# Optimization experiments

Hardware: AMD Instinct MI355X
Metric: run time of the kernel (lower is better)

## Reference

```python
import jax, jax.numpy as jnp
import numpy as np
from jax import lax

N, C, K = 400000, 64, 27  # points, channels, 3x3x3 kernel offsets


def setup_inputs() -> dict:
    key = jax.random.key(0)
    ks = jax.random.split(key, 7)
    scale = 1.0 / np.sqrt(C * K)
    x = jax.random.normal(ks[0], (N, C), dtype=jnp.float32)
    W0 = jax.random.normal(ks[1], (K, C, C), dtype=jnp.float32) * scale
    b0 = jax.random.normal(ks[2], (C,), dtype=jnp.float32) * 0.01
    W1 = jax.random.normal(ks[3], (K, C, C), dtype=jnp.float32) * scale
    b1 = jax.random.normal(ks[4], (C,), dtype=jnp.float32) * 0.01
    # stride-1 conv: input/output coordinate sets coincide -> shared neighbor map
    neighbor_idx = jax.random.randint(ks[5], (N, K), 0, N, dtype=jnp.int32)
    neighbor_mask = jax.random.bernoulli(ks[6], 0.5, (N, K))  # bool, missing neighbors masked
    return {"x": x, "W0": W0, "b0": b0, "W1": W1, "b1": b1,
            "neighbor_idx": neighbor_idx, "neighbor_mask": neighbor_mask}


def _sparse_conv(x, W, b, neighbor_idx, neighbor_mask):
    # gather-GEMM-scatter, accumulated over the K=27 kernel offsets via scan
    # x: [N,C], W: [K,C,C], neighbor_idx/mask: [N,K]
    def body(acc, inputs):
        w_k, idx_k, m_k = inputs  # [C,C], [N], [N]
        g = x[idx_k] * m_k.astype(x.dtype)[:, None]  # masked gather [N,C]
        return acc + g @ w_k, None

    acc0 = jnp.zeros_like(x)
    acc, _ = lax.scan(body, acc0, (W, neighbor_idx.T, neighbor_mask.T))
    return acc + b


def reference(x, W0, b0, W1, b1, neighbor_idx, neighbor_mask):
    out = jax.nn.relu(_sparse_conv(x, W0, b0, neighbor_idx, neighbor_mask))
    out = _sparse_conv(out, W1, b1, neighbor_idx, neighbor_mask)
    return out + x  # residual add
```

## Files before the change

### kernel.cpp

```cpp
#include <hip/hip_runtime.h>
#include <stdint.h>

typedef __attribute__((ext_vector_type(8))) short short8;
typedef __attribute__((ext_vector_type(4))) float floatx4;
typedef __attribute__((ext_vector_type(4))) int int4v;
typedef __attribute__((ext_vector_type(4))) short short4v;

#define NPTS 400000
#define KOFF 27

__device__ __forceinline__ unsigned short f2bf(float v) {
    union { float f; unsigned int u; } a; a.f = v;
    unsigned int r = a.u + 0x7FFFu + ((a.u >> 16) & 1u);
    return (unsigned short)(r >> 16);
}

__global__ __launch_bounds__(256) void cvt_x_kernel(const float* __restrict__ x,
                                                    unsigned short* __restrict__ xb,
                                                    int n4) {
    int t = blockIdx.x * 256 + threadIdx.x;
    if (t >= n4) return;
    floatx4 v = *(const floatx4*)(x + (size_t)t * 4);
    short4v o;
#pragma unroll
    for (int j = 0; j < 4; ++j) o[j] = (short)f2bf(v[j]);
    *(short4v*)(xb + (size_t)t * 4) = o;
}

__global__ __launch_bounds__(256) void pack_kernel(const int* __restrict__ idx,
                                                   const int* __restrict__ msk,
                                                   int* __restrict__ pk, int n4) {
    int t = blockIdx.x * 256 + threadIdx.x;
    if (t >= n4) return;
    int4v a = *(const int4v*)(idx + (size_t)t * 4);
    int4v m = *(const int4v*)(msk + (size_t)t * 4);
    int4v o;
#pragma unroll
    for (int j = 0; j < 4; ++j) o[j] = a[j] | (m[j] ? (int)0x80000000 : 0);
    *(int4v*)(pk + (size_t)t * 4) = o;
}

__global__ __launch_bounds__(256) void cvt_w_kernel(const float* __restrict__ W,
                                                    unsigned short* __restrict__ wb) {
    int t = blockIdx.x * 256 + threadIdx.x;
    int k = t >> 12, cout = (t >> 6) & 63, cin = t & 63;
    wb[t] = f2bf(W[(k << 12) + (cin << 6) + cout]);
}

template <int LAYER>
__global__ __launch_bounds__(256, 4) void conv_layer(
        const unsigned short* __restrict__ xb,
        const unsigned short* __restrict__ wb,
        const float* __restrict__ bias,
        const int* __restrict__ pk,
        const float* __restrict__ xres,
        unsigned short* __restrict__ ob,
        float* __restrict__ outf) {
    const int tid = threadIdx.x;
    const int wv = tid >> 6, lane = tid & 63;
    const int row = lane & 15, kg = lane >> 4;
    const int base = blockIdx.x * 128 + wv * 32;
    const int pr0 = (base + row) * KOFF;
    const int pr1 = (base + 16 + row) * KOFF;

    floatx4 acc[2][4];
#pragma unroll
    for (int mt = 0; mt < 2; ++mt)
#pragma unroll
        for (int nt = 0; nt < 4; ++nt) acc[mt][nt] = (floatx4)0.0f;

    short8 Ac[2][2], An[2][2];
    int pg[2], pl[2] = {0, 0};

    pg[0] = pk[pr0];
    pg[1] = pk[pr1];
#pragma unroll
    for (int mt = 0; mt < 2; ++mt) {
        Ac[mt][0] = (short8)0; Ac[mt][1] = (short8)0;
        if (pg[mt] < 0) {
            const unsigned short* p = xb + ((size_t)(pg[mt] & 0x7FFFFFFF) << 6) + (kg << 3);
            Ac[mt][0] = *(const short8*)p;
            Ac[mt][1] = *(const short8*)(p + 32);
        }
    }
    pg[0] = pk[pr0 + 1];
    pg[1] = pk[pr1 + 1];

#pragma unroll
    for (int k = 0; k < KOFF; ++k) {
        if (k < KOFF - 1) {
#pragma unroll
            for (int mt = 0; mt < 2; ++mt) {
                An[mt][0] = (short8)0; An[mt][1] = (short8)0;
                if (pg[mt] < 0) {
                    const unsigned short* p = xb + ((size_t)(pg[mt] & 0x7FFFFFFF) << 6) + (kg << 3);
                    An[mt][0] = *(const short8*)p;
                    An[mt][1] = *(const short8*)(p + 32);
                }
            }
        }
        if (k < KOFF - 2) {
            pl[0] = pk[pr0 + k + 2];
            pl[1] = pk[pr1 + k + 2];
        }
        const unsigned short* wk = wb + (k << 12);
#pragma unroll
        for (int s = 0; s < 2; ++s) {
#pragma unroll
            for (int nt = 0; nt < 4; ++nt) {
                const short8 b = *(const short8*)(wk + ((nt * 16 + row) << 6) + (s << 5) + (kg << 3));
                acc[0][nt] = __builtin_amdgcn_mfma_f32_16x16x32_bf16(Ac[0][s], b, acc[0][nt], 0, 0, 0);
                acc[1][nt] = __builtin_amdgcn_mfma_f32_16x16x32_bf16(Ac[1][s], b, acc[1][nt], 0, 0, 0);
            }
        }
#pragma unroll
        for (int mt = 0; mt < 2; ++mt) {
            Ac[mt][0] = An[mt][0];
            Ac[mt][1] = An[mt][1];
            pg[mt] = pl[mt];
        }
    }

    const int col = row;
#pragma unroll
    for (int mt = 0; mt < 2; ++mt) {
#pragma unroll
        for (int nt = 0; nt < 4; ++nt) {
            const float bc = bias[nt * 16 + col];
#pragma unroll
            for (int i = 0; i < 4; ++i) {
                const size_t p = base + mt * 16 + kg * 4 + i;
                const int c = nt * 16 + col;
                float v = acc[mt][nt][i] + bc;
                if (LAYER == 0) {
                    ob[p * 64 + c] = f2bf(fmaxf(v, 0.0f));
                } else {
                    outf[p * 64 + c] = v + xres[p * 64 + c];
                }
            }
        }
    }
}

extern "C" void kernel_launch(void* const* d_in, const int* in_sizes, int n_in,
                              void* d_out, int out_size, void* d_ws, size_t ws_size,
                              hipStream_t stream) {
    const float* x  = (const float*)d_in[0];
    const float* W0 = (const float*)d_in[1];
    const float* b0 = (const float*)d_in[2];
    const float* W1 = (const float*)d_in[3];
    const float* b1 = (const float*)d_in[4];
    const int* nidx = (const int*)d_in[5];
    const int* nmask = (const int*)d_in[6];
    float* out = (float*)d_out;

    char* ws = (char*)d_ws;
    const size_t rowBytes = (size_t)NPTS * 64 * sizeof(short);
    const size_t pkBytes  = (size_t)NPTS * KOFF * sizeof(int);
    const size_t wBytes   = (size_t)KOFF * 64 * 64 * sizeof(short);
    unsigned short* xb = (unsigned short*)(ws);
    unsigned short* hb = (unsigned short*)(ws + rowBytes);
    int* pkbuf         = (int*)(ws + 2 * rowBytes);
    unsigned short* w0b = (unsigned short*)(ws + 2 * rowBytes + pkBytes);
    unsigned short* w1b = (unsigned short*)(ws + 2 * rowBytes + pkBytes + wBytes);

    cvt_x_kernel<<<25000, 256, 0, stream>>>(x, xb, NPTS * 64 / 4);
    pack_kernel<<<10547, 256, 0, stream>>>(nidx, nmask, pkbuf, NPTS * KOFF / 4);
    cvt_w_kernel<<<432, 256, 0, stream>>>(W0, w0b);
    cvt_w_kernel<<<432, 256, 0, stream>>>(W1, w1b);

    conv_layer<0><<<3125, 256, 0, stream>>>(xb, w0b, b0, pkbuf, nullptr, hb, nullptr);
    conv_layer<1><<<3125, 256, 0, stream>>>(hb, w1b, b1, pkbuf, x, nullptr, out);
}
```

Before: 1.131 ms.

## Deepen gather prefetch to three offsets ahead with a four-slot register ring

Replaces the single-stage double buffer of gathered neighbor rows with a four-slot register ring that keeps gathers three kernel offsets ahead, and prefetches packed indices six offsets ahead. Weight fragments for both K halves are loaded up front and a sched_barrier separates the loads from the MFMA block. The aim is to hide the latency of random global gathers behind more in-flight loads. In exchange, register pressure rises, so launch bounds drop from 4 to 3 blocks per CU, which lowers occupancy.

```diff
diff --git a/kernel.cpp b/kernel.cpp
--- a/kernel.cpp
+++ b/kernel.cpp
@@ -48,7 +48,7 @@
 }
 
 template <int LAYER>
-__global__ __launch_bounds__(256, 4) void conv_layer(
+__global__ __launch_bounds__(256, 3) void conv_layer(
         const unsigned short* __restrict__ xb,
         const unsigned short* __restrict__ wb,
         const float* __restrict__ bias,
@@ -62,6 +62,7 @@
     const int base = blockIdx.x * 128 + wv * 32;
     const int pr0 = (base + row) * KOFF;
     const int pr1 = (base + 16 + row) * KOFF;
+    const int aoff = kg << 3;
 
     floatx4 acc[2][4];
 #pragma unroll
@@ -69,57 +70,60 @@
 #pragma unroll
         for (int nt = 0; nt < 4; ++nt) acc[mt][nt] = (floatx4)0.0f;
 
-    short8 Ac[2][2], An[2][2];
-    int pg[2], pl[2] = {0, 0};
+    short8 A[4][2][2];
 
-    pg[0] = pk[pr0];
-    pg[1] = pk[pr1];
-#pragma unroll
-    for (int mt = 0; mt < 2; ++mt) {
-        Ac[mt][0] = (short8)0; Ac[mt][1] = (short8)0;
-        if (pg[mt] < 0) {
-            const unsigned short* p = xb + ((size_t)(pg[mt] & 0x7FFFFFFF) << 6) + (kg << 3);
-            Ac[mt][0] = *(const short8*)p;
-            Ac[mt][1] = *(const short8*)(p + 32);
-        }
+#define GATHER(buf, q0, q1) do { \
+    (buf)[0][0] = (short8)0; (buf)[0][1] = (short8)0; \
+    (buf)[1][0] = (short8)0; (buf)[1][1] = (short8)0; \
+    if ((q0) < 0) { \
+        const unsigned short* p_ = xb + ((size_t)((q0) & 0x7FFFFFFF) << 6) + aoff; \
+        (buf)[0][0] = *(const short8*)p_; (buf)[0][1] = *(const short8*)(p_ + 32); } \
+    if ((q1) < 0) { \
+        const unsigned short* p_ = xb + ((size_t)((q1) & 0x7FFFFFFF) << 6) + aoff; \
+        (buf)[1][0] = *(const short8*)p_; (buf)[1][1] = *(const short8*)(p_ + 32); } \
+  } while (0)
+
+    {
+        int q0 = pk[pr0 + 0], q1 = pk[pr1 + 0];
+        GATHER(A[0], q0, q1);
+        q0 = pk[pr0 + 1]; q1 = pk[pr1 + 1];
+        GATHER(A[1], q0, q1);
+        q0 = pk[pr0 + 2]; q1 = pk[pr1 + 2];
+        GATHER(A[2], q0, q1);
     }
-    pg[0] = pk[pr0 + 1];
-    pg[1] = pk[pr1 + 1];
+    int pgA0 = pk[pr0 + 3], pgA1 = pk[pr1 + 3];
+    int pgB0 = pk[pr0 + 4], pgB1 = pk[pr1 + 4];
+    int pgC0 = pk[pr0 + 5], pgC1 = pk[pr1 + 5];
 
 #pragma unroll
     for (int k = 0; k < KOFF; ++k) {
-        if (k < KOFF - 1) {
+        const unsigned short* wk = wb + (k << 12);
+        short8 b0[4], b1[4];
 #pragma unroll
-            for (int mt = 0; mt < 2; ++mt) {
-                An[mt][0] = (short8)0; An[mt][1] = (short8)0;
-                if (pg[mt] < 0) {
-                    const unsigned short* p = xb + ((size_t)(pg[mt] & 0x7FFFFFFF) << 6) + (kg << 3);
-                    An[mt][0] = *(const short8*)p;
-                    An[mt][1] = *(const short8*)(p + 32);
-                }
-            }
-        }
-        if (k < KOFF - 2) {
-            pl[0] = pk[pr0 + k + 2];
-            pl[1] = pk[pr1 + k + 2];
-        }
-        const unsigned short* wk = wb + (k << 12);
+        for (int nt = 0; nt < 4; ++nt)
+            b0[nt] = *(const short8*)(wk + ((nt * 16 + row) << 6) + (kg << 3));
 #pragma unroll
-        for (int s = 0; s < 2; ++s) {
+        for (int nt = 0; nt < 4; ++nt)
+            b1[nt] = *(const short8*)(wk + ((nt * 16 + row) << 6) + 32 + (kg << 3));
+        if (k + 3 < KOFF) GATHER(A[(k + 3) & 3], pgA0, pgA1);
+        int pl0 = 0, pl1 = 0;
+        if (k + 6 < KOFF) { pl0 = pk[pr0 + k + 6]; pl1 = pk[pr1 + k + 6]; }
+        __builtin_amdgcn_sched_barrier(0);
 #pragma unroll
-            for (int nt = 0; nt < 4; ++nt) {
-                const short8 b = *(const short8*)(wk + ((nt * 16 + row) << 6) + (s << 5) + (kg << 3));
-                acc[0][nt] = __builtin_amdgcn_mfma_f32_16x16x32_bf16(Ac[0][s], b, acc[0][nt], 0, 0, 0);
-                acc[1][nt] = __builtin_amdgcn_mfma_f32_16x16x32_bf16(Ac[1][s], b, acc[1][nt], 0, 0, 0);
-            }
+        for (int nt = 0; nt < 4; ++nt) {
+            acc[0][nt] = __builtin_amdgcn_mfma_f32_16x16x32_bf16(A[k & 3][0][0], b0[nt], acc[0][nt], 0, 0, 0);
+            acc[1][nt] = __builtin_amdgcn_mfma_f32_16x16x32_bf16(A[k & 3][1][0], b0[nt], acc[1][nt], 0, 0, 0);
         }
 #pragma unroll
-        for (int mt = 0; mt < 2; ++mt) {
-            Ac[mt][0] = An[mt][0];
-            Ac[mt][1] = An[mt][1];
-            pg[mt] = pl[mt];
+        for (int nt = 0; nt < 4; ++nt) {
+            acc[0][nt] = __builtin_amdgcn_mfma_f32_16x16x32_bf16(A[k & 3][0][1], b1[nt], acc[0][nt], 0, 0, 0);
+            acc[1][nt] = __builtin_amdgcn_mfma_f32_16x16x32_bf16(A[k & 3][1][1], b1[nt], acc[1][nt], 0, 0, 0);
         }
+        pgA0 = pgB0; pgA1 = pgB1;
+        pgB0 = pgC0; pgB1 = pgC1;
+        pgC0 = pl0;  pgC1 = pl1;
     }
+#undef GATHER
 
     const int col = row;
 #pragma unroll
```

Result: slower. 1.178 ms (+4.2%).
